# Kernel tuning notes

Measured on AMD Instinct MI355X. Metric: run time of the kernel, lower is better.

## Reference

```python
import jax, jax.numpy as jnp
import numpy as np

DOT_THRESHOLD = 0.9995  # fall back to normalized lerp when quats nearly parallel
EPS = 1e-8


def _normalize(q, axis=-1):
    return q / jnp.clip(jnp.linalg.norm(q, axis=axis, keepdims=True), 1e-12)


def _quaternion_slerp(q0, q1, t):
    """Batched slerp. q0,q1: (N,4); t: (N,). Standard shortest-arc slerp."""
    dot = jnp.sum(q0 * q1, axis=-1)
    q1 = jnp.where(dot[..., None] < 0.0, -q1, q1)  # take shortest path
    dot = jnp.clip(jnp.abs(dot), -1.0, 1.0)
    theta = jnp.arccos(dot)
    sin_theta = jnp.sin(theta)
    safe_sin = jnp.where(sin_theta < EPS, 1.0, sin_theta)
    s0 = jnp.sin((1.0 - t) * theta) / safe_sin
    s1 = jnp.sin(t * theta) / safe_sin
    slerped = s0[..., None] * q0 + s1[..., None] * q1
    # near-parallel fallback: normalized linear interpolation
    lerped = _normalize(q0 + t[..., None] * (q1 - q0))
    return jnp.where(dot[..., None] > DOT_THRESHOLD, lerped, slerped)


def setup_inputs() -> dict:
    key = jax.random.key(0)
    k1, k2, k3 = jax.random.split(key, 3)
    N = 8_388_608  # number of time samples
    K = 64         # num_keyframes
    t = jax.random.uniform(k1, (N,), dtype=jnp.float32)
    translations = jax.random.normal(k2, (K, 3), dtype=jnp.float32) * 0.1
    quaternions = jax.random.normal(k3, (K, 4), dtype=jnp.float32)
    quaternions = quaternions.at[:, 0].add(2.0)  # bias toward identity like init
    keyframe_times = jnp.linspace(0.0, 1.0, K, dtype=jnp.float32)
    return {"t": t, "translations": translations, "quaternions": quaternions,
            "keyframe_times": keyframe_times}


def reference(t, translations, quaternions, keyframe_times):
    quats = _normalize(quaternions)  # F.normalize(self.quaternions, dim=-1)
    K = keyframe_times.shape[0]
    orig_shape = t.shape
    tf = t.reshape(-1)  # (N,)

    idx = jnp.searchsorted(keyframe_times, tf)  # left, matches torch default
    idx = jnp.clip(idx, 1, K - 1)
    idx_prev = idx - 1

    t_prev = keyframe_times[idx_prev]
    t_next = keyframe_times[idx]
    local_t = (tf - t_prev) / (t_next - t_prev + 1e-8)  # (N,)

    trans_prev = translations[idx_prev]  # (N,3)
    trans_next = translations[idx]
    quat_prev = quats[idx_prev]          # (N,4)
    quat_next = quats[idx]

    trans = (1.0 - local_t)[..., None] * trans_prev + local_t[..., None] * trans_next
    quat = _quaternion_slerp(quat_prev, quat_next, local_t)

    return trans.reshape(*orig_shape, 3), quat.reshape(*orig_shape, 4)
```

## Files before the change

### kernel.cpp

```cpp
#include <hip/hip_runtime.h>
#include <math.h>


#define KFR 64
#define BLOCK 256

__global__ __launch_bounds__(BLOCK) void temporal_motor_kernel(
    const float* __restrict__ t_in,
    const float* __restrict__ translations,
    const float* __restrict__ quaternions,
    const float* __restrict__ keyframe_times,
    float* __restrict__ out_trans,
    float* __restrict__ out_quat,
    int n4)
{
    __shared__ float4 s_q[KFR];
    __shared__ float4 s_t[KFR];

    const int tid = threadIdx.x;
    if (tid < KFR) {
        float qx = quaternions[4 * tid + 0];
        float qy = quaternions[4 * tid + 1];
        float qz = quaternions[4 * tid + 2];
        float qw = quaternions[4 * tid + 3];
        float nrm = sqrtf(qx * qx + qy * qy + qz * qz + qw * qw);
        float inv = 1.0f / fmaxf(nrm, 1e-12f);
        s_q[tid] = make_float4(qx * inv, qy * inv, qz * inv, qw * inv);
        s_t[tid] = make_float4(translations[3 * tid + 0],
                               translations[3 * tid + 1],
                               translations[3 * tid + 2],
                               keyframe_times[tid]);
    }
    __syncthreads();

    const float4* __restrict__ t4 = (const float4*)t_in;
    const int stride = gridDim.x * blockDim.x;

    for (int i = blockIdx.x * blockDim.x + tid; i < n4; i += stride) {
        float4 tv = t4[i];

        float trx[4], try_[4], trz[4];
        float4 oq[4];

        #pragma unroll
        for (int j = 0; j < 4; ++j) {
            float tt = (j == 0) ? tv.x : (j == 1) ? tv.y : (j == 2) ? tv.z : tv.w;

            int g = (int)ceilf(tt * (float)(KFR - 1));
            g = (g < 1) ? 1 : (g > KFR - 1) ? KFR - 1 : g;
            float4 tp = s_t[g - 1];
            float4 tn = s_t[g];
            while (g > 1 && tp.w >= tt) { --g; tn = tp; tp = s_t[g - 1]; }
            while (g < KFR - 1 && tn.w < tt) { ++g; tp = tn; tn = s_t[g]; }

            float lt  = (tt - tp.w) / (tn.w - tp.w + 1e-8f);
            float omt = 1.0f - lt;

            trx[j] = omt * tp.x + lt * tn.x;
            try_[j] = omt * tp.y + lt * tn.y;
            trz[j] = omt * tp.z + lt * tn.z;

            float4 q0 = s_q[g - 1];
            float4 q1 = s_q[g];
            float d = q0.x * q1.x + q0.y * q1.y + q0.z * q1.z + q0.w * q1.w;
            float sgn = (d < 0.0f) ? -1.0f : 1.0f;
            q1.x *= sgn; q1.y *= sgn; q1.z *= sgn; q1.w *= sgn;
            d = fminf(fabsf(d), 1.0f);

            float theta = acosf(d);
            float st2   = fmaxf(1.0f - d * d, 0.0f);
            float st    = sqrtf(st2);
            float invst = (st < 1e-8f) ? 1.0f : (1.0f / st);

            float s0 = __sinf(omt * theta) * invst;
            float s1 = __sinf(lt * theta) * invst;

            float sx = s0 * q0.x + s1 * q1.x;
            float sy = s0 * q0.y + s1 * q1.y;
            float sz = s0 * q0.z + s1 * q1.z;
            float sw = s0 * q0.w + s1 * q1.w;

            float lx = q0.x + lt * (q1.x - q0.x);
            float ly = q0.y + lt * (q1.y - q0.y);
            float lz = q0.z + lt * (q1.z - q0.z);
            float lw = q0.w + lt * (q1.w - q0.w);
            float ln = sqrtf(lx * lx + ly * ly + lz * lz + lw * lw);
            float li = 1.0f / fmaxf(ln, 1e-12f);

            bool fb = (d > 0.9995f);
            oq[j] = fb ? make_float4(lx * li, ly * li, lz * li, lw * li)
                       : make_float4(sx, sy, sz, sw);
        }

        float4* ot = (float4*)(out_trans + (size_t)i * 12);
        ot[0] = make_float4(trx[0], try_[0], trz[0], trx[1]);
        ot[1] = make_float4(try_[1], trz[1], trx[2], try_[2]);
        ot[2] = make_float4(trz[2], trx[3], try_[3], trz[3]);

        float4* oqp = (float4*)(out_quat + (size_t)i * 16);
        oqp[0] = oq[0]; oqp[1] = oq[1]; oqp[2] = oq[2]; oqp[3] = oq[3];
    }
}

__global__ void temporal_motor_tail(
    const float* __restrict__ t_in,
    const float* __restrict__ translations,
    const float* __restrict__ quaternions,
    const float* __restrict__ keyframe_times,
    float* __restrict__ out_trans,
    float* __restrict__ out_quat,
    int n_start, int n)
{
    int i = n_start + blockIdx.x * blockDim.x + threadIdx.x;
    if (i >= n) return;
    float tt = t_in[i];

    int g = 1;
    while (g < KFR - 1 && keyframe_times[g] < tt) ++g;
    float tpw = keyframe_times[g - 1], tnw = keyframe_times[g];
    float lt = (tt - tpw) / (tnw - tpw + 1e-8f);
    float omt = 1.0f - lt;

    for (int c = 0; c < 3; ++c)
        out_trans[3 * (size_t)i + c] =
            omt * translations[3 * (g - 1) + c] + lt * translations[3 * g + c];

    float q0[4], q1[4];
    float n0 = 0, n1 = 0;
    for (int c = 0; c < 4; ++c) { q0[c] = quaternions[4 * (g - 1) + c]; n0 += q0[c] * q0[c]; }
    for (int c = 0; c < 4; ++c) { q1[c] = quaternions[4 * g + c];       n1 += q1[c] * q1[c]; }
    float i0 = 1.0f / fmaxf(sqrtf(n0), 1e-12f), i1 = 1.0f / fmaxf(sqrtf(n1), 1e-12f);
    float d = 0;
    for (int c = 0; c < 4; ++c) { q0[c] *= i0; q1[c] *= i1; }
    for (int c = 0; c < 4; ++c) d += q0[c] * q1[c];
    float sgn = (d < 0.0f) ? -1.0f : 1.0f;
    for (int c = 0; c < 4; ++c) q1[c] *= sgn;
    d = fminf(fabsf(d), 1.0f);
    float theta = acosf(d);
    float st = sqrtf(fmaxf(1.0f - d * d, 0.0f));
    float invst = (st < 1e-8f) ? 1.0f : (1.0f / st);
    float s0 = __sinf(omt * theta) * invst, s1 = __sinf(lt * theta) * invst;
    float l[4], ln = 0;
    for (int c = 0; c < 4; ++c) { l[c] = q0[c] + lt * (q1[c] - q0[c]); ln += l[c] * l[c]; }
    float li = 1.0f / fmaxf(sqrtf(ln), 1e-12f);
    bool fb = (d > 0.9995f);
    for (int c = 0; c < 4; ++c)
        out_quat[4 * (size_t)i + c] = fb ? l[c] * li : (s0 * q0[c] + s1 * q1[c]);
}

extern "C" void kernel_launch(void* const* d_in, const int* in_sizes, int n_in,
                              void* d_out, int out_size, void* d_ws, size_t ws_size,
                              hipStream_t stream) {
    const float* t_in  = (const float*)d_in[0];
    const float* trans = (const float*)d_in[1];
    const float* quats = (const float*)d_in[2];
    const float* ktime = (const float*)d_in[3];
    const int N = in_sizes[0];

    float* out_trans = (float*)d_out;
    float* out_quat  = (float*)d_out + (size_t)N * 3;

    const int n4 = N / 4;
    int blocks = (n4 + BLOCK - 1) / BLOCK;
    if (blocks > 2048) blocks = 2048;
    if (blocks < 1) blocks = 1;

    if (n4 > 0)
        temporal_motor_kernel<<<blocks, BLOCK, 0, stream>>>(
            t_in, trans, quats, ktime, out_trans, out_quat, n4);

    const int rem_start = n4 * 4;
    if (rem_start < N) {
        int rem = N - rem_start;
        temporal_motor_tail<<<(rem + 63) / 64, 64, 0, stream>>>(
            t_in, trans, quats, ktime, out_trans, out_quat, rem_start, N);
    }
}
```

Before: 301.4 us.

## Precompute per-segment slerp constants and switch to lane-contiguous element mapping

Keyframe-segment quantities (theta, 1/sin theta, dot, sign-fixed normalized quaternions, translation deltas, inverse segment length) are now computed once per block into shared memory, so the per-sample work shrinks to one sincos and a few FMAs. The lerp normalization is computed analytically from the dot product rather than from a per-sample vector norm. The access pattern changes from four consecutive elements per thread with float4 loads and stores to four strided elements per thread, each with a scalar load and float3/float4 stores. The kernel is memory bound, so the ALU savings may matter little, and the new store pattern could coalesce worse than before.

```diff
diff --git a/kernel.cpp b/kernel.cpp
--- a/kernel.cpp
+++ b/kernel.cpp
@@ -2,8 +2,10 @@
 #include <math.h>
 
 
-#define KFR 64
+#define KFR   64
+#define NSEG  63
 #define BLOCK 256
+#define CHUNK 1024
 
 __global__ __launch_bounds__(BLOCK) void temporal_motor_kernel(
     const float* __restrict__ t_in,
@@ -12,93 +14,105 @@
     const float* __restrict__ keyframe_times,
     float* __restrict__ out_trans,
     float* __restrict__ out_quat,
-    int n4)
+    int nchunks)
 {
-    __shared__ float4 s_q[KFR];
-    __shared__ float4 s_t[KFR];
+    __shared__ float4 sA[KFR];
+    __shared__ float4 sB[KFR];
+    __shared__ float4 sC[KFR];
+    __shared__ float4 sQ0[KFR];
+    __shared__ float4 sQ1[KFR];
 
     const int tid = threadIdx.x;
-    if (tid < KFR) {
-        float qx = quaternions[4 * tid + 0];
-        float qy = quaternions[4 * tid + 1];
-        float qz = quaternions[4 * tid + 2];
-        float qw = quaternions[4 * tid + 3];
-        float nrm = sqrtf(qx * qx + qy * qy + qz * qz + qw * qw);
-        float inv = 1.0f / fmaxf(nrm, 1e-12f);
-        s_q[tid] = make_float4(qx * inv, qy * inv, qz * inv, qw * inv);
-        s_t[tid] = make_float4(translations[3 * tid + 0],
-                               translations[3 * tid + 1],
-                               translations[3 * tid + 2],
-                               keyframe_times[tid]);
+    if (tid < NSEG) {
+        const int s = tid;
+        float t0 = keyframe_times[s];
+        float t1 = keyframe_times[s + 1];
+
+        float ax = quaternions[4 * s + 0], ay = quaternions[4 * s + 1];
+        float az = quaternions[4 * s + 2], aw = quaternions[4 * s + 3];
+        float bx = quaternions[4 * s + 4], by = quaternions[4 * s + 5];
+        float bz = quaternions[4 * s + 6], bw = quaternions[4 * s + 7];
+        float ia = 1.0f / fmaxf(sqrtf(ax * ax + ay * ay + az * az + aw * aw), 1e-12f);
+        float ib = 1.0f / fmaxf(sqrtf(bx * bx + by * by + bz * bz + bw * bw), 1e-12f);
+        ax *= ia; ay *= ia; az *= ia; aw *= ia;
+        bx *= ib; by *= ib; bz *= ib; bw *= ib;
+
+        float d0 = ax * bx + ay * by + az * bz + aw * bw;
+        float sgn = (d0 < 0.0f) ? -1.0f : 1.0f;
+        bx *= sgn; by *= sgn; bz *= sgn; bw *= sgn;
+        float d = fminf(fabsf(d0), 1.0f);
+
+        float theta = acosf(d);
+        float st    = sqrtf(fmaxf(1.0f - d * d, 0.0f));
+        float inv_st = (d > 0.9995f) ? 0.0f : (1.0f / st);
+
+        float px = translations[3 * s + 0], py = translations[3 * s + 1];
+        float pz = translations[3 * s + 2];
+        float nx = translations[3 * s + 3], ny = translations[3 * s + 4];
+        float nz = translations[3 * s + 5];
+
+        sA[s]  = make_float4(t0, t1, 1.0f / (t1 - t0 + 1e-8f), theta);
+        sB[s]  = make_float4(px, py, pz, inv_st);
+        sC[s]  = make_float4(nx - px, ny - py, nz - pz, d);
+        sQ0[s] = make_float4(ax, ay, az, aw);
+        sQ1[s] = make_float4(bx, by, bz, bw);
     }
     __syncthreads();
 
-    const float4* __restrict__ t4 = (const float4*)t_in;
-    const int stride = gridDim.x * blockDim.x;
+    const int lane = tid & 63;
+    const int wave = tid >> 6;
 
-    for (int i = blockIdx.x * blockDim.x + tid; i < n4; i += stride) {
-        float4 tv = t4[i];
-
-        float trx[4], try_[4], trz[4];
-        float4 oq[4];
+    for (int chunk = blockIdx.x; chunk < nchunks; chunk += gridDim.x) {
+        const int base = chunk * CHUNK + wave * 256 + lane;
 
         #pragma unroll
         for (int j = 0; j < 4; ++j) {
-            float tt = (j == 0) ? tv.x : (j == 1) ? tv.y : (j == 2) ? tv.z : tv.w;
+            const int idx = base + j * 64;
+            const float tt = t_in[idx];
 
-            int g = (int)ceilf(tt * (float)(KFR - 1));
-            g = (g < 1) ? 1 : (g > KFR - 1) ? KFR - 1 : g;
-            float4 tp = s_t[g - 1];
-            float4 tn = s_t[g];
-            while (g > 1 && tp.w >= tt) { --g; tn = tp; tp = s_t[g - 1]; }
-            while (g < KFR - 1 && tn.w < tt) { ++g; tp = tn; tn = s_t[g]; }
+            int s = (int)ceilf(tt * (float)NSEG) - 1;
+            s = (s < 0) ? 0 : (s > NSEG - 1) ? NSEG - 1 : s;
+            float4 a = sA[s];
+            while (s > 0 && a.x >= tt)        { --s; a = sA[s]; }
+            while (s < NSEG - 1 && a.y < tt)  { ++s; a = sA[s]; }
 
-            float lt  = (tt - tp.w) / (tn.w - tp.w + 1e-8f);
-            float omt = 1.0f - lt;
+            const float lt  = (tt - a.x) * a.z;
+            const float omt = 1.0f - lt;
 
-            trx[j] = omt * tp.x + lt * tn.x;
-            try_[j] = omt * tp.y + lt * tn.y;
-            trz[j] = omt * tp.z + lt * tn.z;
+            const float4 b = sB[s];
+            const float4 c = sC[s];
 
-            float4 q0 = s_q[g - 1];
-            float4 q1 = s_q[g];
-            float d = q0.x * q1.x + q0.y * q1.y + q0.z * q1.z + q0.w * q1.w;
-            float sgn = (d < 0.0f) ? -1.0f : 1.0f;
-            q1.x *= sgn; q1.y *= sgn; q1.z *= sgn; q1.w *= sgn;
-            d = fminf(fabsf(d), 1.0f);
+            float3 tr;
+            tr.x = fmaf(lt, c.x, b.x);
+            tr.y = fmaf(lt, c.y, b.y);
+            tr.z = fmaf(lt, c.z, b.z);
 
-            float theta = acosf(d);
-            float st2   = fmaxf(1.0f - d * d, 0.0f);
-            float st    = sqrtf(st2);
-            float invst = (st < 1e-8f) ? 1.0f : (1.0f / st);
+            float sn, cs;
+            __sincosf(lt * a.w, &sn, &cs);
+            const float d   = c.w;
+            const float wbs = sn * b.w;
+            const float was = cs - d * wbs;
 
-            float s0 = __sinf(omt * theta) * invst;
-            float s1 = __sinf(lt * theta) * invst;
+            const float s2  = fmaf(-2.0f * lt * omt, 1.0f - d, 1.0f);
+            const float inv = rsqrtf(fmaxf(s2, 1e-24f));
+            const float wal = omt * inv;
+            const float wbl = lt * inv;
 
-            float sx = s0 * q0.x + s1 * q1.x;
-            float sy = s0 * q0.y + s1 * q1.y;
-            float sz = s0 * q0.z + s1 * q1.z;
-            float sw = s0 * q0.w + s1 * q1.w;
+            const bool fb = (d > 0.9995f);
+            const float wa = fb ? wal : was;
+            const float wb = fb ? wbl : wbs;
 
-            float lx = q0.x + lt * (q1.x - q0.x);
-            float ly = q0.y + lt * (q1.y - q0.y);
-            float lz = q0.z + lt * (q1.z - q0.z);
-            float lw = q0.w + lt * (q1.w - q0.w);
-            float ln = sqrtf(lx * lx + ly * ly + lz * lz + lw * lw);
-            float li = 1.0f / fmaxf(ln, 1e-12f);
+            const float4 q0 = sQ0[s];
+            const float4 q1 = sQ1[s];
+            float4 oq;
+            oq.x = wa * q0.x + wb * q1.x;
+            oq.y = wa * q0.y + wb * q1.y;
+            oq.z = wa * q0.z + wb * q1.z;
+            oq.w = wa * q0.w + wb * q1.w;
 
-            bool fb = (d > 0.9995f);
-            oq[j] = fb ? make_float4(lx * li, ly * li, lz * li, lw * li)
-                       : make_float4(sx, sy, sz, sw);
+            *(float3*)(out_trans + (size_t)idx * 3) = tr;
+            *(float4*)(out_quat  + (size_t)idx * 4) = oq;
         }
-
-        float4* ot = (float4*)(out_trans + (size_t)i * 12);
-        ot[0] = make_float4(trx[0], try_[0], trz[0], trx[1]);
-        ot[1] = make_float4(try_[1], trz[1], trx[2], try_[2]);
-        ot[2] = make_float4(trz[2], trx[3], try_[3], trz[3]);
-
-        float4* oqp = (float4*)(out_quat + (size_t)i * 16);
-        oqp[0] = oq[0]; oqp[1] = oq[1]; oqp[2] = oq[2]; oqp[3] = oq[3];
     }
 }
 
@@ -109,14 +123,14 @@
     const float* __restrict__ keyframe_times,
     float* __restrict__ out_trans,
     float* __restrict__ out_quat,
-    int n_start, int n)
+    int n_start, int n, int K)
 {
     int i = n_start + blockIdx.x * blockDim.x + threadIdx.x;
     if (i >= n) return;
     float tt = t_in[i];
 
     int g = 1;
-    while (g < KFR - 1 && keyframe_times[g] < tt) ++g;
+    while (g < K - 1 && keyframe_times[g] < tt) ++g;
     float tpw = keyframe_times[g - 1], tnw = keyframe_times[g];
     float lt = (tt - tpw) / (tnw - tpw + 1e-8f);
     float omt = 1.0f - lt;
@@ -156,23 +170,26 @@
     const float* quats = (const float*)d_in[2];
     const float* ktime = (const float*)d_in[3];
     const int N = in_sizes[0];
+    const int K = in_sizes[3];
 
     float* out_trans = (float*)d_out;
     float* out_quat  = (float*)d_out + (size_t)N * 3;
 
-    const int n4 = N / 4;
-    int blocks = (n4 + BLOCK - 1) / BLOCK;
-    if (blocks > 2048) blocks = 2048;
-    if (blocks < 1) blocks = 1;
-
-    if (n4 > 0)
-        temporal_motor_kernel<<<blocks, BLOCK, 0, stream>>>(
-            t_in, trans, quats, ktime, out_trans, out_quat, n4);
-
-    const int rem_start = n4 * 4;
-    if (rem_start < N) {
-        int rem = N - rem_start;
-        temporal_motor_tail<<<(rem + 63) / 64, 64, 0, stream>>>(
-            t_in, trans, quats, ktime, out_trans, out_quat, rem_start, N);
+    if (K == KFR) {
+        const int nchunks = N / CHUNK;
+        if (nchunks > 0) {
+            int blocks = nchunks < 2048 ? nchunks : 2048;
+            temporal_motor_kernel<<<blocks, BLOCK, 0, stream>>>(
+                t_in, trans, quats, ktime, out_trans, out_quat, nchunks);
+        }
+        const int rem_start = nchunks * CHUNK;
+        if (rem_start < N) {
+            int rem = N - rem_start;
+            temporal_motor_tail<<<(rem + 63) / 64, 64, 0, stream>>>(
+                t_in, trans, quats, ktime, out_trans, out_quat, rem_start, N, K);
+        }
+    } else {
+        temporal_motor_tail<<<(N + 255) / 256, 256, 0, stream>>>(
+            t_in, trans, quats, ktime, out_trans, out_quat, 0, N, K);
     }
 }
```

Measured after the change: 262.4 us. 1.15x faster.
